# Optimization experiments

Hardware: AMD Instinct MI355X
Metric: run time of the kernel (lower is better)

## Reference

```python
import jax, jax.numpy as jnp
import numpy as np

B, C_IN, C_OUT, H, W, K = 64, 64, 128, 64, 64, 3


def setup_inputs() -> dict:
    key = jax.random.key(0)
    k1, k2, k3 = jax.random.split(key, 3)
    x = jax.random.normal(k1, (B, C_IN, H, W), dtype=jnp.float32)
    weight = jax.random.normal(k2, (C_OUT, C_IN, K, K), dtype=jnp.float32)
    bias = jax.random.normal(k3, (C_OUT, 1, 1), dtype=jnp.float32)
    return {"x": x, "weight": weight, "bias": bias}


def reference(x, weight, bias):
    # Valid (no pad), stride-1, NCHW direct conv + broadcast bias, matching
    # the naive nested-loop conv2d_multi_in_out + bias of MyConv2D.
    out = jax.lax.conv_general_dilated(
        x, weight,
        window_strides=(1, 1),
        padding="VALID",
        dimension_numbers=("NCHW", "OIHW", "NCHW"),
    )
    return out + bias  # bias (C_out,1,1) broadcasts over (B, C_out, H_out, W_out)
```

## Files before the change

kernel.cpp:

```cpp
#include <hip/hip_runtime.h>

#define CI 64
#define CO 128
#define HH 64
#define WW 64
#define OH 62
#define OW 62
#define XTW 66
#define RB (XTW * 64)
#define ROWS_OUT 4
#define ROWS_IN 6
#define NBLK_X 16

typedef __attribute__((ext_vector_type(8))) short short8x;
typedef __attribute__((ext_vector_type(16))) float f32x16;

__device__ __attribute__((aligned(16))) ushort g_wt[9 * CO * CI];

__device__ __forceinline__ ushort bf16rne(float f) {
    unsigned u = __builtin_bit_cast(unsigned, f);
    u += 0x7fffu + ((u >> 16) & 1u);
    return (ushort)(u >> 16);
}

__global__ __launch_bounds__(256)
void wprep(const float* __restrict__ w) {
    const int idx = blockIdx.x * 256 + threadIdx.x;
    const int kk = idx >> 13;
    const int rem = idx & 8191;
    const int co = rem >> 6, ci = rem & 63;
    g_wt[idx] = bf16rne(w[(co * 64 + ci) * 9 + kk]);
}

__global__ __launch_bounds__(256, 2)
void conv_fused(const float* __restrict__ x, const float* __restrict__ bias,
                float* __restrict__ out) {
    __shared__ ushort Xl[ROWS_IN * RB];
    __shared__ float  sB[CO];

    const int tid = threadIdx.x;
    const int wv = tid >> 6, L = tid & 63, l31 = L & 31, q = L >> 5;
    const int h = wv >> 1;
    const int rw = wv & 1;
    const int b = blockIdx.y, oh0 = blockIdx.x * ROWS_OUT;

    if (tid < CO) sB[tid] = bias[tid];

    const ushort* wbase = g_wt + (h * 64 + l31) * 64 + q * 8;
    short8x wbuf[2][8];
    #pragma unroll
    for (int m = 0; m < 2; ++m)
        #pragma unroll
        for (int ss = 0; ss < 4; ++ss)
            wbuf[0][m * 4 + ss] = *(const short8x*)(wbase + m * 2048 + ss * 16);

    if (tid < 96) {
        const int r6 = tid >> 4, c = tid & 15;
        const int px = 64 + (c >> 3), slot = c & 7;
        const uint4 z{0, 0, 0, 0};
        *reinterpret_cast<uint4*>(&Xl[(r6 * XTW + px) * 64 + slot * 8]) = z;
    }

    {
        const int w = L;
        const size_t cibase = (size_t)(b * 64 + wv * 16) * (HH * WW);
        #pragma unroll
        for (int r6 = 0; r6 < ROWS_IN; ++r6) {
            int ir = oh0 + r6;
            if (ir > 63) ir = 63;
            const float* src = x + cibase + (size_t)ir * WW + w;
            union { ushort u[8]; uint4 v; } p0, p1;
            #pragma unroll
            for (int k = 0; k < 8; ++k)
                p0.u[k] = bf16rne(src[(size_t)k * (HH * WW)]);
            #pragma unroll
            for (int k = 0; k < 8; ++k)
                p1.u[k] = bf16rne(src[(size_t)(8 + k) * (HH * WW)]);
            const int pl = r6 * XTW + w, key = pl & 7;
            ushort* dst = &Xl[pl * 64];
            *reinterpret_cast<uint4*>(dst + (((2 * wv)     ^ key) * 8)) = p0.v;
            *reinterpret_cast<uint4*>(dst + (((2 * wv + 1) ^ key) * 8)) = p1.v;
        }
    }

    f32x16 acc[2][2][2];
    #pragma unroll
    for (int r2 = 0; r2 < 2; ++r2)
        #pragma unroll
        for (int i = 0; i < 2; ++i)
            #pragma unroll
            for (int jj = 0; jj < 2; ++jj)
                #pragma unroll
                for (int r = 0; r < 16; ++r) acc[r2][i][jj][r] = 0.f;

    __syncthreads();

    #pragma unroll
    for (int kk = 0; kk < 9; ++kk) {
        const short8x* wf = wbuf[kk & 1];
        if (kk < 8) {
            const ushort* nb = wbase + (kk + 1) * (CO * CI);
            #pragma unroll
            for (int m = 0; m < 2; ++m)
                #pragma unroll
                for (int ss = 0; ss < 4; ++ss)
                    wbuf[(kk + 1) & 1][m * 4 + ss] = *(const short8x*)(nb + m * 2048 + ss * 16);
        }
        const int kr = kk / 3, kc = kk - kr * 3;
        const int pBa = (rw + kr) * XTW + kc + l31;
        const int pBb = (rw + 2 + kr) * XTW + kc + l31;
        const ushort* bPa = Xl + pBa * 64;
        const ushort* bPb = Xl + pBb * 64;
        const int f0a = pBa & 7, f0b = pBb & 7;
        #pragma unroll
        for (int ss = 0; ss < 4; ++ss) {
            const int oba = (((ss * 2 + q) ^ f0a) * 8);
            const int obb = (((ss * 2 + q) ^ f0b) * 8);
            short8x a0 = *(const short8x*)(bPa + oba);
            short8x a1 = *(const short8x*)(bPa + 32 * 64 + oba);
            short8x c0 = *(const short8x*)(bPb + obb);
            short8x c1 = *(const short8x*)(bPb + 32 * 64 + obb);
            acc[0][0][0] = __builtin_amdgcn_mfma_f32_32x32x16_bf16(wf[ss],     a0, acc[0][0][0], 0, 0, 0);
            acc[0][0][1] = __builtin_amdgcn_mfma_f32_32x32x16_bf16(wf[ss],     a1, acc[0][0][1], 0, 0, 0);
            acc[0][1][0] = __builtin_amdgcn_mfma_f32_32x32x16_bf16(wf[4 + ss], a0, acc[0][1][0], 0, 0, 0);
            acc[0][1][1] = __builtin_amdgcn_mfma_f32_32x32x16_bf16(wf[4 + ss], a1, acc[0][1][1], 0, 0, 0);
            acc[1][0][0] = __builtin_amdgcn_mfma_f32_32x32x16_bf16(wf[ss],     c0, acc[1][0][0], 0, 0, 0);
            acc[1][0][1] = __builtin_amdgcn_mfma_f32_32x32x16_bf16(wf[ss],     c1, acc[1][0][1], 0, 0, 0);
            acc[1][1][0] = __builtin_amdgcn_mfma_f32_32x32x16_bf16(wf[4 + ss], c0, acc[1][1][0], 0, 0, 0);
            acc[1][1][1] = __builtin_amdgcn_mfma_f32_32x32x16_bf16(wf[4 + ss], c1, acc[1][1][1], 0, 0, 0);
        }
    }

    #pragma unroll
    for (int r2 = 0; r2 < 2; ++r2) {
        const int oh = oh0 + rw + 2 * r2;
        if (oh < OH) {
            #pragma unroll
            for (int mt = 0; mt < 2; ++mt)
                #pragma unroll
                for (int nt = 0; nt < 2; ++nt) {
                    const int col = nt * 32 + l31;
                    if (col < OW) {
                        #pragma unroll
                        for (int reg = 0; reg < 16; ++reg) {
                            const int co = h * 64 + mt * 32 + 4 * q + (reg & 3) + 8 * (reg >> 2);
                            out[(((size_t)b * CO + co) * OH + oh) * OW + col] = acc[r2][mt][nt][reg] + sB[co];
                        }
                    }
                }
        }
    }
}

extern "C" void kernel_launch(void* const* d_in, const int* in_sizes, int n_in,
                              void* d_out, int out_size, void* d_ws, size_t ws_size,
                              hipStream_t stream) {
    const float* x    = (const float*)d_in[0];
    const float* wgt  = (const float*)d_in[1];
    const float* bias = (const float*)d_in[2];
    float* out = (float*)d_out;

    wprep<<<dim3(288), 256, 0, stream>>>(wgt);
    conv_fused<<<dim3(NBLK_X, 64), 256, 0, stream>>>(x, bias, out);
}
```

Measured before the change: 217.2 us.

## Overlap loading of last two input rows with first kernel-row MFMAs

The input staging is split. Only the first four input rows are converted and written to LDS before the first barrier. The last two rows are loaded from global memory into registers while the MFMAs for kernel row 0 run, then converted and stored, followed by a second barrier before kernel rows 1 and 2. This is meant to hide global load latency behind compute, at the cost of 32 extra live float registers per thread and an extra barrier, which could reduce occupancy or cause spills.

```diff
diff --git a/kernel.cpp b/kernel.cpp
--- a/kernel.cpp
+++ b/kernel.cpp
@@ -61,26 +61,23 @@
         *reinterpret_cast<uint4*>(&Xl[(r6 * XTW + px) * 64 + slot * 8]) = z;
     }
 
-    {
-        const int w = L;
-        const size_t cibase = (size_t)(b * 64 + wv * 16) * (HH * WW);
-        #pragma unroll
-        for (int r6 = 0; r6 < ROWS_IN; ++r6) {
-            int ir = oh0 + r6;
-            if (ir > 63) ir = 63;
-            const float* src = x + cibase + (size_t)ir * WW + w;
-            union { ushort u[8]; uint4 v; } p0, p1;
-            #pragma unroll
-            for (int k = 0; k < 8; ++k)
-                p0.u[k] = bf16rne(src[(size_t)k * (HH * WW)]);
-            #pragma unroll
-            for (int k = 0; k < 8; ++k)
-                p1.u[k] = bf16rne(src[(size_t)(8 + k) * (HH * WW)]);
-            const int pl = r6 * XTW + w, key = pl & 7;
-            ushort* dst = &Xl[pl * 64];
-            *reinterpret_cast<uint4*>(dst + (((2 * wv)     ^ key) * 8)) = p0.v;
-            *reinterpret_cast<uint4*>(dst + (((2 * wv + 1) ^ key) * 8)) = p1.v;
-        }
+    const int w = L;
+    const size_t cibase = (size_t)(b * 64 + wv * 16) * (HH * WW);
+    #pragma unroll
+    for (int r6 = 0; r6 < 4; ++r6) {
+        const int ir = oh0 + r6;
+        const float* src = x + cibase + (size_t)ir * WW + w;
+        union { ushort u[8]; uint4 v; } p0, p1;
+        #pragma unroll
+        for (int k = 0; k < 8; ++k)
+            p0.u[k] = bf16rne(src[(size_t)k * (HH * WW)]);
+        #pragma unroll
+        for (int k = 0; k < 8; ++k)
+            p1.u[k] = bf16rne(src[(size_t)(8 + k) * (HH * WW)]);
+        const int pl = r6 * XTW + w, key = pl & 7;
+        ushort* dst = &Xl[pl * 64];
+        *reinterpret_cast<uint4*>(dst + (((2 * wv)     ^ key) * 8)) = p0.v;
+        *reinterpret_cast<uint4*>(dst + (((2 * wv + 1) ^ key) * 8)) = p1.v;
     }
 
     f32x16 acc[2][2][2];
@@ -95,10 +92,21 @@
 
     __syncthreads();
 
-    #pragma unroll
-    for (int kk = 0; kk < 9; ++kk) {
+    float v45[2][16];
+    #pragma unroll
+    for (int r2 = 0; r2 < 2; ++r2) {
+        int ir = oh0 + 4 + r2;
+        if (ir > 63) ir = 63;
+        const float* src = x + cibase + (size_t)ir * WW + w;
+        #pragma unroll
+        for (int k = 0; k < 16; ++k)
+            v45[r2][k] = src[(size_t)k * (HH * WW)];
+    }
+
+    #pragma unroll
+    for (int kk = 0; kk < 3; ++kk) {
         const short8x* wf = wbuf[kk & 1];
-        if (kk < 8) {
+        {
             const ushort* nb = wbase + (kk + 1) * (CO * CI);
             #pragma unroll
             for (int m = 0; m < 2; ++m)
@@ -106,9 +114,9 @@
                 for (int ss = 0; ss < 4; ++ss)
                     wbuf[(kk + 1) & 1][m * 4 + ss] = *(const short8x*)(nb + m * 2048 + ss * 16);
         }
-        const int kr = kk / 3, kc = kk - kr * 3;
-        const int pBa = (rw + kr) * XTW + kc + l31;
-        const int pBb = (rw + 2 + kr) * XTW + kc + l31;
+        const int kc = kk;
+        const int pBa = rw * XTW + kc + l31;
+        const int pBb = (rw + 2) * XTW + kc + l31;
         const ushort* bPa = Xl + pBa * 64;
         const ushort* bPb = Xl + pBb * 64;
         const int f0a = pBa & 7, f0b = pBb & 7;
@@ -133,6 +141,57 @@
 
     #pragma unroll
     for (int r2 = 0; r2 < 2; ++r2) {
+        union { ushort u[8]; uint4 v; } p0, p1;
+        #pragma unroll
+        for (int k = 0; k < 8; ++k) p0.u[k] = bf16rne(v45[r2][k]);
+        #pragma unroll
+        for (int k = 0; k < 8; ++k) p1.u[k] = bf16rne(v45[r2][8 + k]);
+        const int pl = (4 + r2) * XTW + w, key = pl & 7;
+        ushort* dst = &Xl[pl * 64];
+        *reinterpret_cast<uint4*>(dst + (((2 * wv)     ^ key) * 8)) = p0.v;
+        *reinterpret_cast<uint4*>(dst + (((2 * wv + 1) ^ key) * 8)) = p1.v;
+    }
+
+    __syncthreads();
+
+    #pragma unroll
+    for (int kk = 3; kk < 9; ++kk) {
+        const short8x* wf = wbuf[kk & 1];
+        if (kk < 8) {
+            const ushort* nb = wbase + (kk + 1) * (CO * CI);
+            #pragma unroll
+            for (int m = 0; m < 2; ++m)
+                #pragma unroll
+                for (int ss = 0; ss < 4; ++ss)
+                    wbuf[(kk + 1) & 1][m * 4 + ss] = *(const short8x*)(nb + m * 2048 + ss * 16);
+        }
+        const int kr = kk / 3, kc = kk - kr * 3;
+        const int pBa = (rw + kr) * XTW + kc + l31;
+        const int pBb = (rw + 2 + kr) * XTW + kc + l31;
+        const ushort* bPa = Xl + pBa * 64;
+        const ushort* bPb = Xl + pBb * 64;
+        const int f0a = pBa & 7, f0b = pBb & 7;
+        #pragma unroll
+        for (int ss = 0; ss < 4; ++ss) {
+            const int oba = (((ss * 2 + q) ^ f0a) * 8);
+            const int obb = (((ss * 2 + q) ^ f0b) * 8);
+            short8x a0 = *(const short8x*)(bPa + oba);
+            short8x a1 = *(const short8x*)(bPa + 32 * 64 + oba);
+            short8x c0 = *(const short8x*)(bPb + obb);
+            short8x c1 = *(const short8x*)(bPb + 32 * 64 + obb);
+            acc[0][0][0] = __builtin_amdgcn_mfma_f32_32x32x16_bf16(wf[ss],     a0, acc[0][0][0], 0, 0, 0);
+            acc[0][0][1] = __builtin_amdgcn_mfma_f32_32x32x16_bf16(wf[ss],     a1, acc[0][0][1], 0, 0, 0);
+            acc[0][1][0] = __builtin_amdgcn_mfma_f32_32x32x16_bf16(wf[4 + ss], a0, acc[0][1][0], 0, 0, 0);
+            acc[0][1][1] = __builtin_amdgcn_mfma_f32_32x32x16_bf16(wf[4 + ss], a1, acc[0][1][1], 0, 0, 0);
+            acc[1][0][0] = __builtin_amdgcn_mfma_f32_32x32x16_bf16(wf[ss],     c0, acc[1][0][0], 0, 0, 0);
+            acc[1][0][1] = __builtin_amdgcn_mfma_f32_32x32x16_bf16(wf[ss],     c1, acc[1][0][1], 0, 0, 0);
+            acc[1][1][0] = __builtin_amdgcn_mfma_f32_32x32x16_bf16(wf[4 + ss], c0, acc[1][1][0], 0, 0, 0);
+            acc[1][1][1] = __builtin_amdgcn_mfma_f32_32x32x16_bf16(wf[4 + ss], c1, acc[1][1][1], 0, 0, 0);
+        }
+    }
+
+    #pragma unroll
+    for (int r2 = 0; r2 < 2; ++r2) {
         const int oh = oh0 + rw + 2 * r2;
         if (oh < OH) {
             #pragma unroll
```

After: 214.9 us. Within noise of the previous version (-1.1%).
